# Performance work log

Measured on AMD Instinct MI355X. Metric: run time of the kernel, lower is better.

Reference implementation:

```python
import jax, jax.numpy as jnp
import numpy as np

HIDDEN = 1024
HEADS = 16
HEAD_DIM = HIDDEN // HEADS
SEG_VOCAB = 100


def setup_inputs() -> dict:
    key = jax.random.key(0)
    ks = jax.random.split(key, 12)
    B, T, S = 4, 512, 4096
    s = 1.0 / np.sqrt(HIDDEN)
    return {
        "query": jax.random.normal(ks[0], (B, T, HIDDEN), jnp.float32),
        "key": jax.random.normal(ks[1], (B, S, HIDDEN), jnp.float32),
        "value": jax.random.normal(ks[2], (B, S, HIDDEN), jnp.float32),
        "attention_mask": jnp.ones((B, S), jnp.int32),
        "segment_ids": jax.random.randint(ks[3], (B, S), 0, SEG_VOCAB),
        "Wq": jax.random.normal(ks[4], (HIDDEN, HIDDEN), jnp.float32) * s,
        "bq": jnp.zeros((HIDDEN,), jnp.float32),
        "Wk": jax.random.normal(ks[5], (HIDDEN, HIDDEN), jnp.float32) * s,
        "bk": jnp.zeros((HIDDEN,), jnp.float32),
        "Wv": jax.random.normal(ks[6], (HIDDEN, HIDDEN), jnp.float32) * s,
        "bv": jnp.zeros((HIDDEN,), jnp.float32),
        "Wo": jax.random.normal(ks[7], (HIDDEN, HIDDEN), jnp.float32) * s,
        "bo": jnp.zeros((HIDDEN,), jnp.float32),
        "seg_emb": jax.random.normal(ks[8], (SEG_VOCAB, HIDDEN), jnp.float32) * 0.02,
    }


def reference(query, key, value, attention_mask, segment_ids,
              Wq, bq, Wk, bk, Wv, bv, Wo, bo, seg_emb):
    B, T, _ = query.shape
    S = key.shape[1]
    # projections (dropout is identity in eval mode)
    Q = query @ Wq + bq
    K = key @ Wk + bk + seg_emb[segment_ids]
    V = value @ Wv + bv
    # split heads: [B, H, L, D]
    Q = Q.reshape(B, T, HEADS, HEAD_DIM).transpose(0, 2, 1, 3)
    K = K.reshape(B, S, HEADS, HEAD_DIM).transpose(0, 2, 1, 3)
    V = V.reshape(B, S, HEADS, HEAD_DIM).transpose(0, 2, 1, 3)
    scores = jnp.einsum('bhtd,bhsd->bhts', Q, K) / np.sqrt(HEAD_DIM)
    mask = (attention_mask == 0)[:, None, None, :]  # [B,1,1,S]
    scores = jnp.where(mask, jnp.float32(-1e9), scores)
    weights = jax.nn.softmax(scores, axis=-1)  # [B,H,T,S]
    attended = jnp.einsum('bhts,bhsd->bhtd', weights, V)
    attended = attended.transpose(0, 2, 1, 3).reshape(B, T, HIDDEN)
    attended_output = attended @ Wo + bo
    provenance_scores = weights.mean(axis=1)  # [B,T,S]
    return attended_output, provenance_scores
```

## Files before the change

kernel.cpp:

```cpp
#include <hip/hip_runtime.h>

typedef __bf16 bf16;
typedef __attribute__((ext_vector_type(8))) __bf16 bf16x8;
typedef __attribute__((ext_vector_type(4))) __bf16 bf16x4;
typedef __attribute__((ext_vector_type(4))) float f32x4;
typedef __attribute__((ext_vector_type(8))) short s16x8;

__global__ __launch_bounds__(256) void wtrans(const float* __restrict__ W,
                                              bf16* __restrict__ Th,
                                              bf16* __restrict__ Tl) {
  __shared__ float Ts[64][65];
  int tid = threadIdx.x;
  int k0 = (blockIdx.x & 15) << 6, n0 = (blockIdx.x >> 4) << 6;
  int r = tid >> 2, c0 = (tid & 3) << 4;
#pragma unroll
  for (int j = 0; j < 16; j += 4) {
    f32x4 v = *(const f32x4*)&W[(size_t)(k0 + r) * 1024 + n0 + c0 + j];
#pragma unroll
    for (int q = 0; q < 4; ++q) Ts[r][c0 + j + q] = v[q];
  }
  __syncthreads();
  int nl = tid & 63, kq = (tid >> 6) << 4;
#pragma unroll
  for (int j = 0; j < 16; ++j) {
    float v = Ts[kq + j][nl];
    bf16 hi = (bf16)v;
    bf16 lo = (bf16)(v - (float)hi);
    Th[(size_t)(n0 + nl) * 1024 + k0 + kq + j] = hi;
    Tl[(size_t)(n0 + nl) * 1024 + k0 + kq + j] = lo;
  }
}

template <int OUTM>
__global__ __launch_bounds__(256, 2) void gemm_mfma(
    const float* __restrict__ A, const bf16* __restrict__ WTh,
    const bf16* __restrict__ WTl, const float* __restrict__ bias,
    float* __restrict__ outF, bf16* __restrict__ outH, bf16* __restrict__ outL,
    int M, int mode, const int* __restrict__ segids,
    const float* __restrict__ segemb) {
  __shared__ __align__(16) bf16 Ah[128][40];
  __shared__ __align__(16) bf16 Al[128][40];

  int tid = threadIdx.x;
  int lane = tid & 63, w = tid >> 6;
  int wm = (w & 1) << 6, wn = (w >> 1) << 6;
  int lrow = lane & 15, lkb = (lane >> 4) << 3;
  int bn = blockIdx.x & 7, bm = blockIdx.x >> 3;
  int m0 = bm << 7, n0 = bn << 7;

  int sm = tid & 127, skb = (tid >> 7) << 4;

  f32x4 acc[4][4];
#pragma unroll
  for (int i = 0; i < 4; i++)
#pragma unroll
    for (int j = 0; j < 4; j++) {
      acc[i][j][0] = 0.f; acc[i][j][1] = 0.f;
      acc[i][j][2] = 0.f; acc[i][j][3] = 0.f;
    }

  for (int k0 = 0; k0 < 1024; k0 += 32) {
    {
      const float* asrc = A + (size_t)(m0 + sm) * 1024 + k0 + skb;
      float av16[16];
      *(f32x4*)&av16[0] = *(const f32x4*)asrc;
      *(f32x4*)&av16[4] = *(const f32x4*)(asrc + 4);
      *(f32x4*)&av16[8] = *(const f32x4*)(asrc + 8);
      *(f32x4*)&av16[12] = *(const f32x4*)(asrc + 12);
      union { bf16 b[16]; s16x8 v[2]; } hh, ll;
#pragma unroll
      for (int j = 0; j < 16; ++j) {
        float x = av16[j];
        bf16 hi = (bf16)x;
        hh.b[j] = hi;
        ll.b[j] = (bf16)(x - (float)hi);
      }
      *(s16x8*)&Ah[sm][skb] = hh.v[0];
      *(s16x8*)&Ah[sm][skb + 8] = hh.v[1];
      *(s16x8*)&Al[sm][skb] = ll.v[0];
      *(s16x8*)&Al[sm][skb + 8] = ll.v[1];
    }
    __syncthreads();

    s16x8 bh[4], bl[4];
#pragma unroll
    for (int nt = 0; nt < 4; ++nt) {
      size_t bro = (size_t)(n0 + wn + nt * 16 + lrow) * 1024 + k0 + lkb;
      bh[nt] = *(const s16x8*)&WTh[bro];
      bl[nt] = *(const s16x8*)&WTl[bro];
    }
    s16x8 ah[4], al[4];
#pragma unroll
    for (int mt = 0; mt < 4; ++mt) {
      ah[mt] = *(const s16x8*)&Ah[wm + mt * 16 + lrow][lkb];
      al[mt] = *(const s16x8*)&Al[wm + mt * 16 + lrow][lkb];
    }
#pragma unroll
    for (int mt = 0; mt < 4; ++mt)
#pragma unroll
      for (int nt = 0; nt < 4; ++nt) {
        acc[mt][nt] = __builtin_amdgcn_mfma_f32_16x16x32_bf16(
            ah[mt], bh[nt], acc[mt][nt], 0, 0, 0);
        acc[mt][nt] = __builtin_amdgcn_mfma_f32_16x16x32_bf16(
            ah[mt], bl[nt], acc[mt][nt], 0, 0, 0);
        acc[mt][nt] = __builtin_amdgcn_mfma_f32_16x16x32_bf16(
            al[mt], bh[nt], acc[mt][nt], 0, 0, 0);
      }
    __syncthreads();
  }

  int rbase = (lane >> 4) << 2;
#pragma unroll
  for (int mt = 0; mt < 4; ++mt) {
#pragma unroll
    for (int r = 0; r < 4; ++r) {
      int m = m0 + wm + mt * 16 + rbase + r;
      int seg = (mode == 1) ? segids[m] : 0;
#pragma unroll
      for (int nt = 0; nt < 4; ++nt) {
        int n = n0 + wn + nt * 16 + lrow;
        float v = acc[mt][nt][r] + bias[n];
        if (mode == 1) v += segemb[(size_t)seg * 1024 + n];
        size_t o = (size_t)m * 1024 + n;
        if constexpr (OUTM == 0) {
          outF[o] = v;
        } else if constexpr (OUTM == 1) {
          outH[o] = (bf16)v;
        } else {
          bf16 hi = (bf16)v;
          outH[o] = hi;
          outL[o] = (bf16)(v - (float)hi);
        }
      }
    }
  }
}

__global__ __launch_bounds__(256, 3) void qk_mfma(
    const bf16* __restrict__ Qh, const bf16* __restrict__ Ql,
    const bf16* __restrict__ Kh, const bf16* __restrict__ Kl,
    const int* __restrict__ mask, float* __restrict__ Sc,
    int G, int TC, int h0, int tBase) {
  int tid = threadIdx.x;
  int lane = tid & 63, w = tid >> 6;
  int wm = (w & 1) << 6, wn = (w >> 1) << 6;
  int lrow = lane & 15, lkb = (lane >> 4) << 3;
  int tiles_t = TC >> 7;
  int bid = blockIdx.x;
  int rest = bid % (tiles_t * 32);
  int bg = bid / (tiles_t * 32);
  int tm = rest % tiles_t, sn = rest / tiles_t;
  int b = bg / G, g = bg % G, h = h0 + g;
  int t0 = tBase + (tm << 7), s0 = sn << 7;
  int tl0 = t0 - tBase + bg * TC;

  f32x4 acc[4][4];
#pragma unroll
  for (int i = 0; i < 4; i++)
#pragma unroll
    for (int j = 0; j < 4; j++) {
      acc[i][j][0] = 0.f; acc[i][j][1] = 0.f;
      acc[i][j][2] = 0.f; acc[i][j][3] = 0.f;
    }

#pragma unroll
  for (int ks = 0; ks < 2; ++ks) {
    s16x8 ah[4], al[4], bh[4], bl[4];
#pragma unroll
    for (int mt = 0; mt < 4; ++mt) {
      size_t ro = (((size_t)((b << 9) + t0 + wm + mt * 16 + lrow)) << 10) +
                  (h << 6) + ks * 32 + lkb;
      ah[mt] = *(const s16x8*)&Qh[ro];
      al[mt] = *(const s16x8*)&Ql[ro];
    }
#pragma unroll
    for (int nt = 0; nt < 4; ++nt) {
      size_t ro = (((size_t)((b << 12) + s0 + wn + nt * 16 + lrow)) << 10) +
                  (h << 6) + ks * 32 + lkb;
      bh[nt] = *(const s16x8*)&Kh[ro];
      bl[nt] = *(const s16x8*)&Kl[ro];
    }
#pragma unroll
    for (int mt = 0; mt < 4; ++mt)
#pragma unroll
      for (int nt = 0; nt < 4; ++nt) {
        acc[mt][nt] = __builtin_amdgcn_mfma_f32_16x16x32_bf16(
            ah[mt], bh[nt], acc[mt][nt], 0, 0, 0);
        acc[mt][nt] = __builtin_amdgcn_mfma_f32_16x16x32_bf16(
            ah[mt], bl[nt], acc[mt][nt], 0, 0, 0);
        acc[mt][nt] = __builtin_amdgcn_mfma_f32_16x16x32_bf16(
            al[mt], bh[nt], acc[mt][nt], 0, 0, 0);
      }
  }

  const int* mrow = mask + (b << 12) + s0 + wn;
  bool mk[4];
#pragma unroll
  for (int nt = 0; nt < 4; ++nt) mk[nt] = (mrow[nt * 16 + lrow] != 0);

  int rbase = (lane >> 4) << 2;
#pragma unroll
  for (int mt = 0; mt < 4; ++mt) {
#pragma unroll
    for (int r = 0; r < 4; ++r) {
      size_t row = (((size_t)(tl0 + wm + mt * 16 + rbase + r)) << 12) + s0 + wn;
#pragma unroll
      for (int nt = 0; nt < 4; ++nt) {
        Sc[row + nt * 16 + lrow] =
            mk[nt] ? acc[mt][nt][r] * 0.125f : -1.0e9f;
      }
    }
  }
}

template <int PMODE>
__global__ __launch_bounds__(256, 2) void softmax_prov(
    float* __restrict__ Sc, bf16* __restrict__ Pb, float* __restrict__ prov,
    int G, int TC, int h0, int tBase) {
  __shared__ float red[4];

  int tid = threadIdx.x, wv = tid >> 6;
  int bid = blockIdx.x;
  int b = bid / TC, tl = bid % TC;
  int t = tBase + tl;

  float pacc[16];
#pragma unroll
  for (int i = 0; i < 16; i++) pacc[i] = 0.f;

  for (int g = 0; g < G; ++g) {
    size_t base = ((size_t)((b * G + g) * TC + tl)) << 12;
    f32x4 v[4];
    float mx = -3.0e38f;
#pragma unroll
    for (int it = 0; it < 4; ++it) {
      int s = (tid << 2) + (it << 10);
      v[it] = *(const f32x4*)&Sc[base + s];
      mx = fmaxf(fmaxf(fmaxf(mx, v[it][0]), v[it][1]), fmaxf(v[it][2], v[it][3]));
    }
#pragma unroll
    for (int o = 32; o; o >>= 1) mx = fmaxf(mx, __shfl_xor(mx, o));
    if ((tid & 63) == 0) red[wv] = mx;
    __syncthreads();
    float m = fmaxf(fmaxf(red[0], red[1]), fmaxf(red[2], red[3]));
    __syncthreads();

    float sm = 0.f;
#pragma unroll
    for (int it = 0; it < 4; ++it) {
      f32x4 p;
      p[0] = __expf(v[it][0] - m);
      p[1] = __expf(v[it][1] - m);
      p[2] = __expf(v[it][2] - m);
      p[3] = __expf(v[it][3] - m);
      v[it] = p;
      sm += (p[0] + p[1]) + (p[2] + p[3]);
    }
#pragma unroll
    for (int o = 32; o; o >>= 1) sm += __shfl_xor(sm, o);
    if ((tid & 63) == 0) red[wv] = sm;
    __syncthreads();
    float il = 1.0f / (((red[0] + red[1]) + (red[2] + red[3])));
    __syncthreads();

#pragma unroll
    for (int it = 0; it < 4; ++it) {
      int s = (tid << 2) + (it << 10);
      f32x4 pn;
      pn[0] = v[it][0] * il;
      pn[1] = v[it][1] * il;
      pn[2] = v[it][2] * il;
      pn[3] = v[it][3] * il;
      if constexpr (PMODE == 1) {
        bf16x4 pb;
        pb[0] = (bf16)pn[0]; pb[1] = (bf16)pn[1];
        pb[2] = (bf16)pn[2]; pb[3] = (bf16)pn[3];
        *(bf16x4*)&Pb[base + s] = pb;
      } else {
        *(f32x4*)&Sc[base + s] = pn;
      }
      pacc[it * 4 + 0] += pn[0] * 0.0625f;
      pacc[it * 4 + 1] += pn[1] * 0.0625f;
      pacc[it * 4 + 2] += pn[2] * 0.0625f;
      pacc[it * 4 + 3] += pn[3] * 0.0625f;
    }
  }

  size_t pbase = (((size_t)((b << 9) + t)) << 12);
#pragma unroll
  for (int it = 0; it < 4; ++it) {
    int s = (tid << 2) + (it << 10);
    f32x4 pa;
    pa[0] = pacc[it * 4 + 0]; pa[1] = pacc[it * 4 + 1];
    pa[2] = pacc[it * 4 + 2]; pa[3] = pacc[it * 4 + 3];
    if (h0 != 0) {
      f32x4 old = *(const f32x4*)&prov[pbase + s];
      pa[0] += old[0]; pa[1] += old[1]; pa[2] += old[2]; pa[3] += old[3];
    }
    *(f32x4*)&prov[pbase + s] = pa;
  }
}

template <typename PT, typename VT>
__global__ __launch_bounds__(256, 2) void pv_gemm(
    const PT* __restrict__ P, const VT* __restrict__ Vp,
    float* __restrict__ Oat, int G, int TC, int h0, int tBase) {
  __shared__ __align__(16) float PsT[32][68];
  __shared__ __align__(16) float Vs[32][68];

  int tid = threadIdx.x, tx = tid & 15, ty = tid >> 4;
  int ntt = TC >> 6;
  int bid = blockIdx.x;
  int tt = bid % ntt, bg = bid / ntt;
  int b = bg / G, g = bg % G, h = h0 + g;
  int tl0 = tt << 6;

  int st = tid & 63, sc = (tid >> 6) * 8;
  int vr = tid >> 3, vc = (tid & 7) * 8;

  float acc[4][4];
#pragma unroll
  for (int i = 0; i < 4; i++)
#pragma unroll
    for (int j = 0; j < 4; j++) acc[i][j] = 0.f;

  for (int k0 = 0; k0 < 4096; k0 += 32) {
    {
      const PT* src = P + (((size_t)(bg * TC + tl0 + st)) << 12) + k0 + sc;
      if constexpr (sizeof(PT) == 2) {
        bf16x8 p8 = *(const bf16x8*)src;
#pragma unroll
        for (int j = 0; j < 8; j++) PsT[sc + j][st] = (float)p8[j];
      } else {
        f32x4 p0 = *(const f32x4*)src;
        f32x4 p1 = *(const f32x4*)(src + 4);
#pragma unroll
        for (int j = 0; j < 4; j++) {
          PsT[sc + j][st] = p0[j];
          PsT[sc + 4 + j][st] = p1[j];
        }
      }
    }
    {
      const VT* src = Vp + (((size_t)((b << 12) + k0 + vr)) << 10) + (h << 6) + vc;
      if constexpr (sizeof(VT) == 4) {
        *(f32x4*)&Vs[vr][vc] = *(const f32x4*)src;
        *(f32x4*)&Vs[vr][vc + 4] = *(const f32x4*)(src + 4);
      } else {
        bf16x8 v8 = *(const bf16x8*)src;
#pragma unroll
        for (int j = 0; j < 8; j++) Vs[vr][vc + j] = (float)v8[j];
      }
    }
    __syncthreads();
#pragma unroll
    for (int kk = 0; kk < 32; ++kk) {
      f32x4 av = *(const f32x4*)&PsT[kk][ty * 4];
      f32x4 bv = *(const f32x4*)&Vs[kk][tx * 4];
#pragma unroll
      for (int i = 0; i < 4; i++)
#pragma unroll
        for (int j = 0; j < 4; j++) acc[i][j] += av[i] * bv[j];
    }
    __syncthreads();
  }

#pragma unroll
  for (int i = 0; i < 4; i++) {
    int t = tBase + tl0 + ty * 4 + i;
    f32x4 v;
#pragma unroll
    for (int j = 0; j < 4; j++) v[j] = acc[i][j];
    *(f32x4*)&Oat[(((size_t)((b << 9) + t)) << 10) + (h << 6) + (tx << 2)] = v;
  }
}

template <typename OUT>
__global__ __launch_bounds__(256, 2) void gemm_f32(
    const float* __restrict__ A, const float* __restrict__ W,
    const float* __restrict__ bias, OUT* __restrict__ out, int M, int mode,
    const int* __restrict__ segids, const float* __restrict__ segemb) {
  __shared__ __align__(16) float AsT[32][132];
  __shared__ __align__(16) float Bs[32][132];

  int tid = threadIdx.x;
  int tx = tid & 15, ty = tid >> 4;
  int nTilesM = M >> 7;
  int bm = blockIdx.x % nTilesM, bn = blockIdx.x / nTilesM;
  int m0 = bm * 128, n0 = bn * 128;

  int sm = tid & 127;
  int skb = (tid >> 7) * 16;

  float acc[8][8];
#pragma unroll
  for (int i = 0; i < 8; i++)
#pragma unroll
    for (int j = 0; j < 8; j++) acc[i][j] = 0.f;

  for (int k0 = 0; k0 < 1024; k0 += 32) {
    {
      const float* src = A + (size_t)(m0 + sm) * 1024 + k0 + skb;
      f32x4 a0 = *(const f32x4*)src;
      f32x4 a1 = *(const f32x4*)(src + 4);
      f32x4 a2 = *(const f32x4*)(src + 8);
      f32x4 a3 = *(const f32x4*)(src + 12);
#pragma unroll
      for (int j = 0; j < 4; j++) {
        AsT[skb + j][sm] = a0[j];
        AsT[skb + 4 + j][sm] = a1[j];
        AsT[skb + 8 + j][sm] = a2[j];
        AsT[skb + 12 + j][sm] = a3[j];
      }
    }
#pragma unroll
    for (int u = tid; u < 512; u += 256) {
      int r = u >> 4, cc = (u & 15) * 8;
      const float* src = W + (size_t)(k0 + r) * 1024 + n0 + cc;
      *(f32x4*)&Bs[r][cc] = *(const f32x4*)src;
      *(f32x4*)&Bs[r][cc + 4] = *(const f32x4*)(src + 4);
    }
    __syncthreads();
#pragma unroll
    for (int kk = 0; kk < 32; kk++) {
      f32x4 av0 = *(const f32x4*)&AsT[kk][ty * 8];
      f32x4 av1 = *(const f32x4*)&AsT[kk][ty * 8 + 4];
      f32x4 bv0 = *(const f32x4*)&Bs[kk][tx * 4];
      f32x4 bv1 = *(const f32x4*)&Bs[kk][64 + tx * 4];
      float av[8] = {av0[0], av0[1], av0[2], av0[3],
                     av1[0], av1[1], av1[2], av1[3]};
#pragma unroll
      for (int i = 0; i < 8; i++) {
#pragma unroll
        for (int j = 0; j < 4; j++) {
          acc[i][j] += av[i] * bv0[j];
          acc[i][4 + j] += av[i] * bv1[j];
        }
      }
    }
    __syncthreads();
  }

#pragma unroll
  for (int i = 0; i < 8; i++) {
    int m = m0 + ty * 8 + i;
    int seg = (mode == 1) ? segids[m] : 0;
#pragma unroll
    for (int jh = 0; jh < 2; jh++) {
#pragma unroll
      for (int j = 0; j < 4; j++) {
        int n = n0 + jh * 64 + tx * 4 + j;
        float v = acc[i][jh * 4 + j] + bias[n];
        if (mode == 1) v += segemb[(size_t)seg * 1024 + n];
        out[(size_t)m * 1024 + n] = (OUT)v;
      }
    }
  }
}

__global__ __launch_bounds__(256) void attn_naive(
    const float* __restrict__ Qp, const float* __restrict__ Kp,
    const bf16* __restrict__ Vp, const int* __restrict__ mask,
    float* __restrict__ Oatt, float* __restrict__ prov) {
  int bt = blockIdx.x;
  int b = bt >> 9, t = bt & 511;
  __shared__ float qs[64];
  __shared__ float sc[4096];
  __shared__ float pacc[4096];
  __shared__ float red[256];
  __shared__ float po[4][64];
  int tid = threadIdx.x, wv = tid >> 6, lane = tid & 63;

  for (int s = tid; s < 4096; s += 256) pacc[s] = 0.f;
  const int* mrow = mask + (b << 12);

  for (int h = 0; h < 16; ++h) {
    __syncthreads();
    if (tid < 64) qs[tid] = Qp[((size_t)(b * 512 + t)) * 1024 + h * 64 + tid];
    __syncthreads();
    for (int s = tid; s < 4096; s += 256) {
      const float* krow = Kp + ((size_t)((b << 12) + s)) * 1024 + h * 64;
      float d = 0.f;
#pragma unroll
      for (int kk = 0; kk < 64; kk += 4) {
        f32x4 kv = *(const f32x4*)(krow + kk);
#pragma unroll
        for (int j = 0; j < 4; ++j) d += qs[kk + j] * kv[j];
      }
      sc[s] = (mrow[s] != 0) ? d * 0.125f : -1.0e9f;
    }
    __syncthreads();
    float mx = -3.0e38f;
    for (int s = tid; s < 4096; s += 256) mx = fmaxf(mx, sc[s]);
    red[tid] = mx;
    __syncthreads();
    for (int off = 128; off; off >>= 1) {
      if (tid < off) red[tid] = fmaxf(red[tid], red[tid + off]);
      __syncthreads();
    }
    float m = red[0];
    __syncthreads();
    float sm = 0.f;
    for (int s = tid; s < 4096; s += 256) {
      float p = __expf(sc[s] - m);
      sc[s] = p;
      sm += p;
    }
    red[tid] = sm;
    __syncthreads();
    for (int off = 128; off; off >>= 1) {
      if (tid < off) red[tid] += red[tid + off];
      __syncthreads();
    }
    float il = 1.0f / red[0];
    for (int s = tid; s < 4096; s += 256) pacc[s] += sc[s] * il * 0.0625f;
    float o = 0.f;
    const bf16* vb = Vp + ((size_t)((b << 12) + wv * 1024)) * 1024 + h * 64 + lane;
    for (int s = 0; s < 1024; ++s) o += sc[wv * 1024 + s] * (float)vb[(size_t)s * 1024];
    po[wv][lane] = o;
    __syncthreads();
    if (tid < 64) {
      float oo = (po[0][tid] + po[1][tid] + po[2][tid] + po[3][tid]) * il;
      Oatt[((size_t)(b * 512 + t)) * 1024 + h * 64 + tid] = oo;
    }
  }
  __syncthreads();
  for (int s = tid; s < 4096; s += 256)
    prov[((size_t)(b * 512 + t)) * 4096 + s] = pacc[s];
}

extern "C" void kernel_launch(void* const* d_in, const int* in_sizes, int n_in,
                              void* d_out, int out_size, void* d_ws, size_t ws_size,
                              hipStream_t stream) {
  const float* query = (const float*)d_in[0];
  const float* key = (const float*)d_in[1];
  const float* value = (const float*)d_in[2];
  const int* amask = (const int*)d_in[3];
  const int* segid = (const int*)d_in[4];
  const float* Wq = (const float*)d_in[5];
  const float* bq = (const float*)d_in[6];
  const float* Wk = (const float*)d_in[7];
  const float* bk = (const float*)d_in[8];
  const float* Wv = (const float*)d_in[9];
  const float* bv = (const float*)d_in[10];
  const float* Wo = (const float*)d_in[11];
  const float* bo = (const float*)d_in[12];
  const float* semb = (const float*)d_in[13];

  char* ws = (char*)d_ws;
  float* outAtt = (float*)d_out;
  float* outProv = outAtt + (size_t)2048 * 1024;

  const size_t MB = 1ull << 20;
  static const int cand[7][2] = {{16, 512}, {8, 512}, {4, 512}, {2, 512},
                                 {1, 512},  {1, 256}, {1, 128}};
  int G = 0, TC = 0;
  size_t scBytes = 0;
  for (int ci = 0; ci < 7; ++ci) {
    size_t sb = (size_t)4 * cand[ci][0] * cand[ci][1] * 4096 * 4;
    if (112 * MB + sb <= ws_size) { G = cand[ci][0]; TC = cand[ci][1]; scBytes = sb; break; }
  }

  if (G > 0) {
    bool vf32 = (144 * MB + scBytes <= ws_size);
    size_t scOff = (vf32 ? 144 : 112) * MB;
    bool usePb = (scOff + scBytes + scBytes / 2 <= ws_size);

    bf16* Qh = (bf16*)ws;
    bf16* Ql = (bf16*)(ws + 4 * MB);
    bf16* Kh = (bf16*)(ws + 8 * MB);
    bf16* Kl = (bf16*)(ws + 40 * MB);
    float* Vpf = (float*)(ws + 72 * MB);
    bf16* Vpb = (bf16*)(ws + 72 * MB);
    float* OatF = (float*)(ws + (vf32 ? 136 : 104) * MB);
    float* Sc = (float*)(ws + scOff);
    bf16* Pb = (bf16*)(ws + scOff + scBytes);
    bf16* WTh = (bf16*)(ws + scOff);
    bf16* WTl = WTh + (size_t)1024 * 1024;

    wtrans<<<256, 256, 0, stream>>>(Wq, WTh, WTl);
    gemm_mfma<2><<<8 * 16, 256, 0, stream>>>(query, WTh, WTl, bq, nullptr, Qh,
                                             Ql, 2048, 0, nullptr, nullptr);
    wtrans<<<256, 256, 0, stream>>>(Wk, WTh, WTl);
    gemm_mfma<2><<<8 * 128, 256, 0, stream>>>(key, WTh, WTl, bk, nullptr, Kh,
                                              Kl, 16384, 1, segid, semb);
    wtrans<<<256, 256, 0, stream>>>(Wv, WTh, WTl);
    if (vf32)
      gemm_mfma<0><<<8 * 128, 256, 0, stream>>>(value, WTh, WTl, bv, Vpf,
                                                nullptr, nullptr, 16384, 0,
                                                nullptr, nullptr);
    else
      gemm_mfma<1><<<8 * 128, 256, 0, stream>>>(value, WTh, WTl, bv, nullptr,
                                                Vpb, nullptr, 16384, 0,
                                                nullptr, nullptr);

    int nHC = 16 / G, nTCk = 512 / TC;
    for (int hc = 0; hc < nHC; ++hc) {
      int h0 = hc * G;
      for (int tc = 0; tc < nTCk; ++tc) {
        int tBase = tc * TC;
        qk_mfma<<<4 * G * (TC >> 7) * 32, 256, 0, stream>>>(
            Qh, Ql, Kh, Kl, amask, Sc, G, TC, h0, tBase);
        if (usePb)
          softmax_prov<1><<<4 * TC, 256, 0, stream>>>(Sc, Pb, outProv, G, TC, h0, tBase);
        else
          softmax_prov<0><<<4 * TC, 256, 0, stream>>>(Sc, Pb, outProv, G, TC, h0, tBase);
        int pvGrid = 4 * G * (TC >> 6);
        if (usePb) {
          if (vf32)
            pv_gemm<bf16, float><<<pvGrid, 256, 0, stream>>>(Pb, Vpf, OatF, G, TC, h0, tBase);
          else
            pv_gemm<bf16, bf16><<<pvGrid, 256, 0, stream>>>(Pb, Vpb, OatF, G, TC, h0, tBase);
        } else {
          if (vf32)
            pv_gemm<float, float><<<pvGrid, 256, 0, stream>>>(Sc, Vpf, OatF, G, TC, h0, tBase);
          else
            pv_gemm<float, bf16><<<pvGrid, 256, 0, stream>>>(Sc, Vpb, OatF, G, TC, h0, tBase);
        }
      }
    }
    wtrans<<<256, 256, 0, stream>>>(Wo, WTh, WTl);
    gemm_mfma<0><<<8 * 16, 256, 0, stream>>>(OatF, WTh, WTl, bo, outAtt,
                                             nullptr, nullptr, 2048, 0,
                                             nullptr, nullptr);
  } else {
    float* Qp = (float*)ws;
    float* Kp = (float*)(ws + 8 * MB);
    bf16* Vp = (bf16*)(ws + 72 * MB);
    float* OatF = (float*)(ws + 104 * MB);

    gemm_f32<float><<<16 * 8, 256, 0, stream>>>(query, Wq, bq, Qp, 2048, 0, nullptr, nullptr);
    gemm_f32<float><<<128 * 8, 256, 0, stream>>>(key, Wk, bk, Kp, 16384, 1, segid, semb);
    gemm_f32<bf16><<<128 * 8, 256, 0, stream>>>(value, Wv, bv, Vp, 16384, 0, nullptr, nullptr);
    attn_naive<<<2048, 256, 0, stream>>>(Qp, Kp, Vp, amask, OatF, outProv);
    gemm_f32<float><<<16 * 8, 256, 0, stream>>>(OatF, Wo, bo, outAtt, 2048, 0, nullptr, nullptr);
  }
}
```

Before: 2.036 ms.

## Move PV product to MFMA with transposed split V, pre-split GEMM inputs

Replaces the scalar FP32 PV GEMM with a bf16 MFMA kernel that reads probabilities in bf16 and a transposed V split into high and low bf16 halves. V is produced in fp32 and then transposed and split by a new kernel. Projection GEMM inputs are pre-split into bf16 hi/lo by a separate pass, so the GEMM reads A directly from global memory without LDS staging or barriers. The workspace layout is fixed to always use the bf16 P path, which costs extra memory traffic for the split buffers and requires a larger workspace.

```diff
diff --git a/kernel.cpp b/kernel.cpp
--- a/kernel.cpp
+++ b/kernel.cpp
@@ -5,6 +5,30 @@
 typedef __attribute__((ext_vector_type(4))) __bf16 bf16x4;
 typedef __attribute__((ext_vector_type(4))) float f32x4;
 typedef __attribute__((ext_vector_type(8))) short s16x8;
+
+__device__ __forceinline__ f32x4 mfma16(s16x8 a, s16x8 b, f32x4 c) {
+  return __builtin_amdgcn_mfma_f32_16x16x32_bf16(a, b, c, 0, 0, 0);
+}
+
+__global__ __launch_bounds__(256) void split_f32(const float* __restrict__ X,
+                                                 bf16* __restrict__ Xh,
+                                                 bf16* __restrict__ Xl,
+                                                 int n4) {
+  int i = blockIdx.x * 256 + threadIdx.x;
+  int stride = gridDim.x * 256;
+  for (; i < n4; i += stride) {
+    f32x4 v = *(const f32x4*)&X[(size_t)i * 4];
+    bf16x4 h, l;
+#pragma unroll
+    for (int j = 0; j < 4; ++j) {
+      bf16 hi = (bf16)v[j];
+      h[j] = hi;
+      l[j] = (bf16)(v[j] - (float)hi);
+    }
+    *(bf16x4*)&Xh[(size_t)i * 4] = h;
+    *(bf16x4*)&Xl[(size_t)i * 4] = l;
+  }
+}
 
 __global__ __launch_bounds__(256) void wtrans(const float* __restrict__ W,
                                               bf16* __restrict__ Th,
@@ -31,16 +55,46 @@
   }
 }
 
+__global__ __launch_bounds__(256) void vtrans(const float* __restrict__ V,
+                                              bf16* __restrict__ Th,
+                                              bf16* __restrict__ Tl) {
+  __shared__ float Ts[64][65];
+  int tid = threadIdx.x;
+  int s0 = (blockIdx.x & 255) << 6;
+  int d0 = (blockIdx.x >> 8) << 6;
+  int r = tid >> 2, c0 = (tid & 3) << 4;
+#pragma unroll
+  for (int j = 0; j < 16; j += 4) {
+    f32x4 v = *(const f32x4*)&V[(size_t)(s0 + r) * 1024 + d0 + c0 + j];
+#pragma unroll
+    for (int q = 0; q < 4; ++q) Ts[r][c0 + j + q] = v[q];
+  }
+  __syncthreads();
+  int d = tid >> 3, sc = (tid & 7) << 3;
+#pragma unroll
+  for (int pass = 0; pass < 2; ++pass) {
+    int dd = d + (pass << 5);
+    union { bf16 b[8]; s16x8 v; } hb, lb;
+#pragma unroll
+    for (int j = 0; j < 8; ++j) {
+      float x = Ts[sc + j][dd];
+      bf16 hi = (bf16)x;
+      hb.b[j] = hi;
+      lb.b[j] = (bf16)(x - (float)hi);
+    }
+    size_t o = (size_t)(d0 + dd) * 16384 + s0 + sc;
+    *(s16x8*)&Th[o] = hb.v;
+    *(s16x8*)&Tl[o] = lb.v;
+  }
+}
+
 template <int OUTM>
 __global__ __launch_bounds__(256, 2) void gemm_mfma(
-    const float* __restrict__ A, const bf16* __restrict__ WTh,
-    const bf16* __restrict__ WTl, const float* __restrict__ bias,
-    float* __restrict__ outF, bf16* __restrict__ outH, bf16* __restrict__ outL,
-    int M, int mode, const int* __restrict__ segids,
-    const float* __restrict__ segemb) {
-  __shared__ __align__(16) bf16 Ah[128][40];
-  __shared__ __align__(16) bf16 Al[128][40];
-
+    const bf16* __restrict__ Ah, const bf16* __restrict__ Al,
+    const bf16* __restrict__ WTh, const bf16* __restrict__ WTl,
+    const float* __restrict__ bias, float* __restrict__ outF,
+    bf16* __restrict__ outH, bf16* __restrict__ outL, int M, int mode,
+    const int* __restrict__ segids, const float* __restrict__ segemb) {
   int tid = threadIdx.x;
   int lane = tid & 63, w = tid >> 6;
   int wm = (w & 1) << 6, wn = (w >> 1) << 6;
@@ -48,8 +102,6 @@
   int bn = blockIdx.x & 7, bm = blockIdx.x >> 3;
   int m0 = bm << 7, n0 = bn << 7;
 
-  int sm = tid & 127, skb = (tid >> 7) << 4;
-
   f32x4 acc[4][4];
 #pragma unroll
   for (int i = 0; i < 4; i++)
@@ -59,54 +111,36 @@
       acc[i][j][2] = 0.f; acc[i][j][3] = 0.f;
     }
 
+  const bf16* aph = Ah + (size_t)(m0 + wm + lrow) * 1024 + lkb;
+  const bf16* apl = Al + (size_t)(m0 + wm + lrow) * 1024 + lkb;
+  const bf16* bph = WTh + (size_t)(n0 + wn + lrow) * 1024 + lkb;
+  const bf16* bpl = WTl + (size_t)(n0 + wn + lrow) * 1024 + lkb;
+
   for (int k0 = 0; k0 < 1024; k0 += 32) {
-    {
-      const float* asrc = A + (size_t)(m0 + sm) * 1024 + k0 + skb;
-      float av16[16];
-      *(f32x4*)&av16[0] = *(const f32x4*)asrc;
-      *(f32x4*)&av16[4] = *(const f32x4*)(asrc + 4);
-      *(f32x4*)&av16[8] = *(const f32x4*)(asrc + 8);
-      *(f32x4*)&av16[12] = *(const f32x4*)(asrc + 12);
-      union { bf16 b[16]; s16x8 v[2]; } hh, ll;
-#pragma unroll
-      for (int j = 0; j < 16; ++j) {
-        float x = av16[j];
-        bf16 hi = (bf16)x;
-        hh.b[j] = hi;
-        ll.b[j] = (bf16)(x - (float)hi);
-      }
-      *(s16x8*)&Ah[sm][skb] = hh.v[0];
-      *(s16x8*)&Ah[sm][skb + 8] = hh.v[1];
-      *(s16x8*)&Al[sm][skb] = ll.v[0];
-      *(s16x8*)&Al[sm][skb + 8] = ll.v[1];
-    }
-    __syncthreads();
-
-    s16x8 bh[4], bl[4];
-#pragma unroll
-    for (int nt = 0; nt < 4; ++nt) {
-      size_t bro = (size_t)(n0 + wn + nt * 16 + lrow) * 1024 + k0 + lkb;
-      bh[nt] = *(const s16x8*)&WTh[bro];
-      bl[nt] = *(const s16x8*)&WTl[bro];
-    }
-    s16x8 ah[4], al[4];
-#pragma unroll
-    for (int mt = 0; mt < 4; ++mt) {
-      ah[mt] = *(const s16x8*)&Ah[wm + mt * 16 + lrow][lkb];
-      al[mt] = *(const s16x8*)&Al[wm + mt * 16 + lrow][lkb];
-    }
+    s16x8 bh[4], ah[4], xl[4];
+#pragma unroll
+    for (int nt = 0; nt < 4; ++nt) bh[nt] = *(const s16x8*)(bph + nt * 16384 + k0);
+#pragma unroll
+    for (int mt = 0; mt < 4; ++mt) ah[mt] = *(const s16x8*)(aph + mt * 16384 + k0);
 #pragma unroll
     for (int mt = 0; mt < 4; ++mt)
 #pragma unroll
-      for (int nt = 0; nt < 4; ++nt) {
-        acc[mt][nt] = __builtin_amdgcn_mfma_f32_16x16x32_bf16(
-            ah[mt], bh[nt], acc[mt][nt], 0, 0, 0);
-        acc[mt][nt] = __builtin_amdgcn_mfma_f32_16x16x32_bf16(
-            ah[mt], bl[nt], acc[mt][nt], 0, 0, 0);
-        acc[mt][nt] = __builtin_amdgcn_mfma_f32_16x16x32_bf16(
-            al[mt], bh[nt], acc[mt][nt], 0, 0, 0);
-      }
-    __syncthreads();
+      for (int nt = 0; nt < 4; ++nt)
+        acc[mt][nt] = mfma16(ah[mt], bh[nt], acc[mt][nt]);
+#pragma unroll
+    for (int mt = 0; mt < 4; ++mt) xl[mt] = *(const s16x8*)(apl + mt * 16384 + k0);
+#pragma unroll
+    for (int mt = 0; mt < 4; ++mt)
+#pragma unroll
+      for (int nt = 0; nt < 4; ++nt)
+        acc[mt][nt] = mfma16(xl[mt], bh[nt], acc[mt][nt]);
+#pragma unroll
+    for (int nt = 0; nt < 4; ++nt) xl[nt] = *(const s16x8*)(bpl + nt * 16384 + k0);
+#pragma unroll
+    for (int mt = 0; mt < 4; ++mt)
+#pragma unroll
+      for (int nt = 0; nt < 4; ++nt)
+        acc[mt][nt] = mfma16(ah[mt], xl[nt], acc[mt][nt]);
   }
 
   int rbase = (lane >> 4) << 2;
@@ -124,8 +158,6 @@
         size_t o = (size_t)m * 1024 + n;
         if constexpr (OUTM == 0) {
           outF[o] = v;
-        } else if constexpr (OUTM == 1) {
-          outH[o] = (bf16)v;
         } else {
           bf16 hi = (bf16)v;
           outH[o] = hi;
@@ -184,12 +216,9 @@
     for (int mt = 0; mt < 4; ++mt)
 #pragma unroll
       for (int nt = 0; nt < 4; ++nt) {
-        acc[mt][nt] = __builtin_amdgcn_mfma_f32_16x16x32_bf16(
-            ah[mt], bh[nt], acc[mt][nt], 0, 0, 0);
-        acc[mt][nt] = __builtin_amdgcn_mfma_f32_16x16x32_bf16(
-            ah[mt], bl[nt], acc[mt][nt], 0, 0, 0);
-        acc[mt][nt] = __builtin_amdgcn_mfma_f32_16x16x32_bf16(
-            al[mt], bh[nt], acc[mt][nt], 0, 0, 0);
+        acc[mt][nt] = mfma16(ah[mt], bh[nt], acc[mt][nt]);
+        acc[mt][nt] = mfma16(ah[mt], bl[nt], acc[mt][nt]);
+        acc[mt][nt] = mfma16(al[mt], bh[nt], acc[mt][nt]);
       }
   }
 
@@ -206,8 +235,7 @@
       size_t row = (((size_t)(tl0 + wm + mt * 16 + rbase + r)) << 12) + s0 + wn;
 #pragma unroll
       for (int nt = 0; nt < 4; ++nt) {
-        Sc[row + nt * 16 + lrow] =
-            mk[nt] ? acc[mt][nt][r] * 0.125f : -1.0e9f;
+        Sc[row + nt * 16 + lrow] = mk[nt] ? acc[mt][nt][r] * 0.125f : -1.0e9f;
       }
     }
   }
@@ -301,77 +329,61 @@
   }
 }
 
-template <typename PT, typename VT>
-__global__ __launch_bounds__(256, 2) void pv_gemm(
-    const PT* __restrict__ P, const VT* __restrict__ Vp,
-    float* __restrict__ Oat, int G, int TC, int h0, int tBase) {
-  __shared__ __align__(16) float PsT[32][68];
-  __shared__ __align__(16) float Vs[32][68];
-
-  int tid = threadIdx.x, tx = tid & 15, ty = tid >> 4;
-  int ntt = TC >> 6;
+__global__ __launch_bounds__(256, 2) void pv_mfma(
+    const bf16* __restrict__ P, const bf16* __restrict__ VTh,
+    const bf16* __restrict__ VTl, float* __restrict__ Oat,
+    int G, int TC, int h0, int tBase) {
+  int tid = threadIdx.x;
+  int lane = tid & 63, w = tid >> 6;
+  int wt0 = w << 5;
+  int lrow = lane & 15, lkb = (lane >> 4) << 3;
+  int ntt = TC >> 7;
   int bid = blockIdx.x;
   int tt = bid % ntt, bg = bid / ntt;
   int b = bg / G, g = bg % G, h = h0 + g;
-  int tl0 = tt << 6;
-
-  int st = tid & 63, sc = (tid >> 6) * 8;
-  int vr = tid >> 3, vc = (tid & 7) * 8;
-
-  float acc[4][4];
-#pragma unroll
-  for (int i = 0; i < 4; i++)
-#pragma unroll
-    for (int j = 0; j < 4; j++) acc[i][j] = 0.f;
+  int tl0 = tt << 7;
+
+  f32x4 acc[2][4];
+#pragma unroll
+  for (int i = 0; i < 2; i++)
+#pragma unroll
+    for (int j = 0; j < 4; j++) {
+      acc[i][j][0] = 0.f; acc[i][j][1] = 0.f;
+      acc[i][j][2] = 0.f; acc[i][j][3] = 0.f;
+    }
+
+  const bf16* pp = P + (((size_t)(bg * TC + tl0 + wt0 + lrow)) << 12) + lkb;
+  const bf16* vph = VTh + (size_t)((h << 6) + lrow) * 16384 + ((size_t)b << 12) + lkb;
+  const bf16* vpl = VTl + (size_t)((h << 6) + lrow) * 16384 + ((size_t)b << 12) + lkb;
 
   for (int k0 = 0; k0 < 4096; k0 += 32) {
-    {
-      const PT* src = P + (((size_t)(bg * TC + tl0 + st)) << 12) + k0 + sc;
-      if constexpr (sizeof(PT) == 2) {
-        bf16x8 p8 = *(const bf16x8*)src;
-#pragma unroll
-        for (int j = 0; j < 8; j++) PsT[sc + j][st] = (float)p8[j];
-      } else {
-        f32x4 p0 = *(const f32x4*)src;
-        f32x4 p1 = *(const f32x4*)(src + 4);
-#pragma unroll
-        for (int j = 0; j < 4; j++) {
-          PsT[sc + j][st] = p0[j];
-          PsT[sc + 4 + j][st] = p1[j];
-        }
-      }
-    }
-    {
-      const VT* src = Vp + (((size_t)((b << 12) + k0 + vr)) << 10) + (h << 6) + vc;
-      if constexpr (sizeof(VT) == 4) {
-        *(f32x4*)&Vs[vr][vc] = *(const f32x4*)src;
-        *(f32x4*)&Vs[vr][vc + 4] = *(const f32x4*)(src + 4);
-      } else {
-        bf16x8 v8 = *(const bf16x8*)src;
-#pragma unroll
-        for (int j = 0; j < 8; j++) Vs[vr][vc + j] = (float)v8[j];
-      }
-    }
-    __syncthreads();
-#pragma unroll
-    for (int kk = 0; kk < 32; ++kk) {
-      f32x4 av = *(const f32x4*)&PsT[kk][ty * 4];
-      f32x4 bv = *(const f32x4*)&Vs[kk][tx * 4];
-#pragma unroll
-      for (int i = 0; i < 4; i++)
-#pragma unroll
-        for (int j = 0; j < 4; j++) acc[i][j] += av[i] * bv[j];
-    }
-    __syncthreads();
-  }
-
-#pragma unroll
-  for (int i = 0; i < 4; i++) {
-    int t = tBase + tl0 + ty * 4 + i;
-    f32x4 v;
-#pragma unroll
-    for (int j = 0; j < 4; j++) v[j] = acc[i][j];
-    *(f32x4*)&Oat[(((size_t)((b << 9) + t)) << 10) + (h << 6) + (tx << 2)] = v;
+    s16x8 pa[2], bvh[4], bvl[4];
+#pragma unroll
+    for (int nt = 0; nt < 4; ++nt) {
+      bvh[nt] = *(const s16x8*)(vph + (size_t)nt * 16 * 16384 + k0);
+      bvl[nt] = *(const s16x8*)(vpl + (size_t)nt * 16 * 16384 + k0);
+    }
+#pragma unroll
+    for (int mt = 0; mt < 2; ++mt) pa[mt] = *(const s16x8*)(pp + mt * (16 * 4096) + k0);
+#pragma unroll
+    for (int mt = 0; mt < 2; ++mt)
+#pragma unroll
+      for (int nt = 0; nt < 4; ++nt) {
+        acc[mt][nt] = mfma16(pa[mt], bvh[nt], acc[mt][nt]);
+        acc[mt][nt] = mfma16(pa[mt], bvl[nt], acc[mt][nt]);
+      }
+  }
+
+  int rbase = (lane >> 4) << 2;
+#pragma unroll
+  for (int mt = 0; mt < 2; ++mt) {
+#pragma unroll
+    for (int r = 0; r < 4; ++r) {
+      int t = tBase + tl0 + wt0 + mt * 16 + rbase + r;
+      size_t obase = (((size_t)((b << 9) + t)) << 10) + (h << 6);
+#pragma unroll
+      for (int nt = 0; nt < 4; ++nt) Oat[obase + nt * 16 + lrow] = acc[mt][nt][r];
+    }
   }
 }
 
@@ -552,47 +564,49 @@
   float* outProv = outAtt + (size_t)2048 * 1024;
 
   const size_t MB = 1ull << 20;
+  const size_t scOff = 144 * MB;
   static const int cand[7][2] = {{16, 512}, {8, 512}, {4, 512}, {2, 512},
                                  {1, 512},  {1, 256}, {1, 128}};
   int G = 0, TC = 0;
   size_t scBytes = 0;
   for (int ci = 0; ci < 7; ++ci) {
     size_t sb = (size_t)4 * cand[ci][0] * cand[ci][1] * 4096 * 4;
-    if (112 * MB + sb <= ws_size) { G = cand[ci][0]; TC = cand[ci][1]; scBytes = sb; break; }
+    size_t need = scOff + sb + sb / 2;
+    size_t scr = scOff + 132 * MB;
+    if (need < scr) need = scr;
+    if (need <= ws_size) { G = cand[ci][0]; TC = cand[ci][1]; scBytes = sb; break; }
   }
 
   if (G > 0) {
-    bool vf32 = (144 * MB + scBytes <= ws_size);
-    size_t scOff = (vf32 ? 144 : 112) * MB;
-    bool usePb = (scOff + scBytes + scBytes / 2 <= ws_size);
-
     bf16* Qh = (bf16*)ws;
     bf16* Ql = (bf16*)(ws + 4 * MB);
     bf16* Kh = (bf16*)(ws + 8 * MB);
     bf16* Kl = (bf16*)(ws + 40 * MB);
-    float* Vpf = (float*)(ws + 72 * MB);
-    bf16* Vpb = (bf16*)(ws + 72 * MB);
-    float* OatF = (float*)(ws + (vf32 ? 136 : 104) * MB);
+    bf16* VTh = (bf16*)(ws + 72 * MB);
+    bf16* VTl = (bf16*)(ws + 104 * MB);
+    float* OatF = (float*)(ws + 136 * MB);
     float* Sc = (float*)(ws + scOff);
     bf16* Pb = (bf16*)(ws + scOff + scBytes);
     bf16* WTh = (bf16*)(ws + scOff);
     bf16* WTl = WTh + (size_t)1024 * 1024;
-
+    bf16* Ash = (bf16*)(ws + scOff + 4 * MB);
+    bf16* Asl = (bf16*)(ws + scOff + 36 * MB);
+    float* Vpf = (float*)(ws + scOff + 68 * MB);
+
+    split_f32<<<2048, 256, 0, stream>>>(query, Ash, Asl, 524288);
     wtrans<<<256, 256, 0, stream>>>(Wq, WTh, WTl);
-    gemm_mfma<2><<<8 * 16, 256, 0, stream>>>(query, WTh, WTl, bq, nullptr, Qh,
-                                             Ql, 2048, 0, nullptr, nullptr);
+    gemm_mfma<2><<<16 * 8, 256, 0, stream>>>(Ash, Asl, WTh, WTl, bq, nullptr,
+                                             Qh, Ql, 2048, 0, nullptr, nullptr);
+    split_f32<<<2048, 256, 0, stream>>>(key, Ash, Asl, 4194304);
     wtrans<<<256, 256, 0, stream>>>(Wk, WTh, WTl);
-    gemm_mfma<2><<<8 * 128, 256, 0, stream>>>(key, WTh, WTl, bk, nullptr, Kh,
-                                              Kl, 16384, 1, segid, semb);
+    gemm_mfma<2><<<128 * 8, 256, 0, stream>>>(Ash, Asl, WTh, WTl, bk, nullptr,
+                                              Kh, Kl, 16384, 1, segid, semb);
+    split_f32<<<2048, 256, 0, stream>>>(value, Ash, Asl, 4194304);
     wtrans<<<256, 256, 0, stream>>>(Wv, WTh, WTl);
-    if (vf32)
-      gemm_mfma<0><<<8 * 128, 256, 0, stream>>>(value, WTh, WTl, bv, Vpf,
-                                                nullptr, nullptr, 16384, 0,
-                                                nullptr, nullptr);
-    else
-      gemm_mfma<1><<<8 * 128, 256, 0, stream>>>(value, WTh, WTl, bv, nullptr,
-                                                Vpb, nullptr, 16384, 0,
-                                                nullptr, nullptr);
+    gemm_mfma<0><<<128 * 8, 256, 0, stream>>>(Ash, Asl, WTh, WTl, bv, Vpf,
+                                              nullptr, nullptr, 16384, 0,
+                                              nullptr, nullptr);
+    vtrans<<<4096, 256, 0, stream>>>(Vpf, VTh, VTl);
 
     int nHC = 16 / G, nTCk = 512 / TC;
     for (int hc = 0; hc < nHC; ++hc) {
@@ -601,26 +615,14 @@
         int tBase = tc * TC;
         qk_mfma<<<4 * G * (TC >> 7) * 32, 256, 0, stream>>>(
             Qh, Ql, Kh, Kl, amask, Sc, G, TC, h0, tBase);
-        if (usePb)
-          softmax_prov<1><<<4 * TC, 256, 0, stream>>>(Sc, Pb, outProv, G, TC, h0, tBase);
-        else
-          softmax_prov<0><<<4 * TC, 256, 0, stream>>>(Sc, Pb, outProv, G, TC, h0, tBase);
-        int pvGrid = 4 * G * (TC >> 6);
-        if (usePb) {
-          if (vf32)
-            pv_gemm<bf16, float><<<pvGrid, 256, 0, stream>>>(Pb, Vpf, OatF, G, TC, h0, tBase);
-          else
-            pv_gemm<bf16, bf16><<<pvGrid, 256, 0, stream>>>(Pb, Vpb, OatF, G, TC, h0, tBase);
-        } else {
-          if (vf32)
-            pv_gemm<float, float><<<pvGrid, 256, 0, stream>>>(Sc, Vpf, OatF, G, TC, h0, tBase);
-          else
-            pv_gemm<float, bf16><<<pvGrid, 256, 0, stream>>>(Sc, Vpb, OatF, G, TC, h0, tBase);
-        }
-      }
-    }
+        softmax_prov<1><<<4 * TC, 256, 0, stream>>>(Sc, Pb, outProv, G, TC, h0, tBase);
+        pv_mfma<<<4 * G * (TC >> 7), 256, 0, stream>>>(Pb, VTh, VTl, OatF, G,
+                                                       TC, h0, tBase);
+      }
+    }
+    split_f32<<<2048, 256, 0, stream>>>(OatF, Ash, Asl, 524288);
     wtrans<<<256, 256, 0, stream>>>(Wo, WTh, WTl);
-    gemm_mfma<0><<<8 * 16, 256, 0, stream>>>(OatF, WTh, WTl, bo, outAtt,
+    gemm_mfma<0><<<16 * 8, 256, 0, stream>>>(Ash, Asl, WTh, WTl, bo, outAtt,
                                              nullptr, nullptr, 2048, 0,
                                              nullptr, nullptr);
   } else {
```

After: 6.326 ms. 3.11x slower.
